# Performance work log

Hardware: AMD Instinct MI355X
Metric: run time of the kernel (lower is better)

## Reference

```python
import jax, jax.numpy as jnp
import numpy as np
from jax.ops import segment_sum, segment_max

N = 38332
E = 1200000
C = 64
POI_LEN = 38333
CAT_LEN = 400
LAYERS = 5


def _glorot(key, shape):
    fan_in, fan_out = shape[0], shape[-1]
    lim = float(np.sqrt(6.0 / (fan_in + fan_out)))
    return jax.random.uniform(key, shape, jnp.float32, -lim, lim)


def gcn_conv(x, src, dst, ew, W, b):
    # PyG GCNConv: x@W, add self-loops (weight 1), symmetric norm, scatter-sum at dst
    h = x @ W  # [N, Cout]
    ar = jnp.arange(N, dtype=src.dtype)
    s = jnp.concatenate([src, ar])
    d = jnp.concatenate([dst, ar])
    w = jnp.concatenate([ew, jnp.ones((N,), ew.dtype)])
    deg = segment_sum(w, d, num_segments=N)
    dinv = jnp.where(deg > 0, jax.lax.rsqrt(jnp.maximum(deg, 1e-12)), 0.0)
    norm = dinv[s] * w * dinv[d]
    out = segment_sum(h[s] * norm[:, None], d, num_segments=N)
    return out + b


def graph_norm(x, w, b, alpha, eps=1e-5):
    mean = jnp.mean(x, axis=0, keepdims=True)
    out = x - alpha * mean
    var = jnp.mean(out * out, axis=0, keepdims=True)
    return out * jax.lax.rsqrt(var + eps) * w + b


def gat_conv(x, src, dst, W, att_src, att_dst, b):
    # PyG GATConv, heads=1, add_self_loops=True, negative_slope=0.2
    h = x @ W  # [N, C]
    ar = jnp.arange(N, dtype=src.dtype)
    s = jnp.concatenate([src, ar])
    d = jnp.concatenate([dst, ar])
    a_s = h @ att_src  # [N]
    a_d = h @ att_dst
    e = jax.nn.leaky_relu(a_s[s] + a_d[d], 0.2)  # [E+N]
    m = segment_max(e, d, num_segments=N)
    ex = jnp.exp(e - m[d])
    z = segment_sum(ex, d, num_segments=N)
    alpha = ex / (z[d] + 1e-16)
    out = segment_sum(h[s] * alpha[:, None], d, num_segments=N)
    return out + b


def setup_inputs() -> dict:
    key = jax.random.key(0)
    ks = jax.random.split(key, 32)
    inp = {
        'poi_idx': jax.random.randint(ks[0], (N,), 0, POI_LEN, jnp.int32),
        'cat_idx': jax.random.randint(ks[1], (N,), 0, CAT_LEN, jnp.int32),
        'feat': jax.random.normal(ks[2], (N, 3), jnp.float32),
        'edge_index': jax.random.randint(ks[3], (2, E), 0, N, jnp.int32),
        'weight': jax.random.uniform(ks[4], (E,), jnp.float32),
        'poi_emb': jax.random.normal(ks[5], (POI_LEN, 300), jnp.float32),
        'cat_emb': jax.random.normal(ks[6], (CAT_LEN, 100), jnp.float32),
        'W_in': _glorot(ks[7], (403, C)),
        'b_in': jnp.zeros((C,), jnp.float32),
        'gcn_W': jax.vmap(lambda k: _glorot(k, (C, C)))(jax.random.split(ks[8], LAYERS)),
        'gcn_b': jnp.zeros((LAYERS, C), jnp.float32),
        'gn_w': jnp.ones((LAYERS, C), jnp.float32),
        'gn_b': jnp.zeros((LAYERS, C), jnp.float32),
        'gn_a': jnp.ones((LAYERS, C), jnp.float32),
        'gat_W': jax.vmap(lambda k: _glorot(k, (C, C)))(jax.random.split(ks[9], LAYERS)),
        'gat_att_src': jax.random.normal(ks[10], (LAYERS, C), jnp.float32) * 0.1,
        'gat_att_dst': jax.random.normal(ks[11], (LAYERS, C), jnp.float32) * 0.1,
        'gat_b': jnp.zeros((LAYERS, C), jnp.float32),
        'W_out': _glorot(ks[12], (C, 1)),
        'b_out': jnp.zeros((1,), jnp.float32),
        'fc1_W': _glorot(ks[13], (N, 128)),
        'fc1_b': jnp.zeros((128,), jnp.float32),
        'fc2_W': _glorot(ks[14], (128, POI_LEN)),
        'fc2_b': jnp.zeros((POI_LEN,), jnp.float32),
    }
    return inp


def reference(poi_idx, cat_idx, feat, edge_index, weight, poi_emb, cat_emb,
              W_in, b_in, gcn_W, gcn_b, gn_w, gn_b, gn_a,
              gat_W, gat_att_src, gat_att_dst, gat_b,
              W_out, b_out, fc1_W, fc1_b, fc2_W, fc2_b):
    src, dst = edge_index[0], edge_index[1]
    lrelu = lambda v: jax.nn.leaky_relu(v, 0.01)  # nn.LeakyReLU default
    x = jnp.concatenate([poi_emb[poi_idx], cat_emb[cat_idx], feat], axis=1)  # [N,403]
    x = lrelu(gcn_conv(x, src, dst, weight, W_in, b_in))  # [N,64]
    for i in range(LAYERS):
        t = gcn_conv(x, src, dst, weight, gcn_W[i], gcn_b[i])
        t = lrelu(graph_norm(t, gn_w[i], gn_b[i], gn_a[i]))
        x = x + t
        t = gat_conv(x, src, dst, gat_W[i], gat_att_src[i], gat_att_dst[i], gat_b[i])
        t = lrelu(graph_norm(t, gn_w[i], gn_b[i], gn_a[i]))
        x = x + t
    x = lrelu(gcn_conv(x, src, dst, weight, W_out, b_out)).reshape(-1)  # [N]
    h = jax.nn.relu(x @ fc1_W + fc1_b)
    out = jax.nn.relu(h @ fc2_W + fc2_b)  # [POI_LEN]
    return out
```

## Files before the change

### kernel.cpp

```cpp
#include <hip/hip_runtime.h>
#include <hip/hip_fp16.h>

#define NN 38332
#define NE 1200000
#define POI 38333
#define NWG 128
#define CHUNK (NE/NWG)
#define SBLK 256
#define FBLK 1024

__device__ __forceinline__ float lrelu01(float v){ return v > 0.f ? v : 0.01f*v; }

__device__ __forceinline__ void load8(const __half* h, int s, int c8, float* f){
  uint4 q = *(const uint4*)((const __half*)h + (size_t)s*64 + c8);
  __half2 h0 = *(__half2*)&q.x, h1 = *(__half2*)&q.y, h2 = *(__half2*)&q.z, h3 = *(__half2*)&q.w;
  float2 r0 = __half22float2(h0), r1 = __half22float2(h1), r2 = __half22float2(h2), r3 = __half22float2(h3);
  f[0]=r0.x; f[1]=r0.y; f[2]=r1.x; f[3]=r1.y; f[4]=r2.x; f[5]=r2.y; f[6]=r3.x; f[7]=r3.y;
}
__device__ __forceinline__ void load8(const float* h, int s, int c8, float* f){
  float4 a = *(const float4*)(h + (size_t)s*64 + c8);
  float4 b = *(const float4*)(h + (size_t)s*64 + c8 + 4);
  f[0]=a.x; f[1]=a.y; f[2]=a.z; f[3]=a.w; f[4]=b.x; f[5]=b.y; f[6]=b.z; f[7]=b.w;
}
__device__ __forceinline__ void store8(float* out, int n, int cb, const float* o){
  *(float4*)&out[(size_t)n*64 + cb]     = make_float4(o[0],o[1],o[2],o[3]);
  *(float4*)&out[(size_t)n*64 + cb + 4] = make_float4(o[4],o[5],o[6],o[7]);
}
__device__ __forceinline__ void store8(__half* out, int n, int cb, const float* o){
  __half2 q0 = __floats2half2_rn(o[0], o[1]);
  __half2 q1 = __floats2half2_rn(o[2], o[3]);
  __half2 q2 = __floats2half2_rn(o[4], o[5]);
  __half2 q3 = __floats2half2_rn(o[6], o[7]);
  uint4 q;
  q.x = *(unsigned*)&q0; q.y = *(unsigned*)&q1; q.z = *(unsigned*)&q2; q.w = *(unsigned*)&q3;
  *(uint4*)((__half*)out + (size_t)n*64 + cb) = q;
}

__global__ __launch_bounds__(1024) void k_hist(const int* __restrict__ dst,
                                               int* __restrict__ partial){
  __shared__ int hist[NN];
  for (int i = threadIdx.x; i < NN; i += 1024) hist[i] = 0;
  __syncthreads();
  int base = blockIdx.x*CHUNK;
  for (int k = threadIdx.x; k < CHUNK; k += 1024)
    atomicAdd(&hist[dst[base + k]], 1);
  __syncthreads();
  for (int i = threadIdx.x; i < NN; i += 1024)
    partial[(size_t)blockIdx.x*NN + i] = hist[i];
}

__global__ __launch_bounds__(256) void k_b1(int* __restrict__ partial, int* __restrict__ counts){
  int bin = blockIdx.x*256 + threadIdx.x;
  if (bin < NN){
    int run = 0;
    for (int wg = 0; wg < NWG; ++wg){
      int v = partial[(size_t)wg*NN + bin];
      partial[(size_t)wg*NN + bin] = run;
      run += v;
    }
    counts[bin] = run;
  }
}

__global__ __launch_bounds__(1024) void k_scan(const int* __restrict__ counts, int* rowptr){
  __shared__ int part[1024];
  int tid = threadIdx.x;
  const int per = (NN + 1023)/1024;
  int base = tid*per;
  int s = 0;
  for (int k = 0; k < per; k++){ int i = base + k; if (i < NN) s += counts[i]; }
  part[tid] = s;
  __syncthreads();
  for (int off = 1; off < 1024; off <<= 1){
    int v = (tid >= off) ? part[tid-off] : 0;
    __syncthreads();
    part[tid] += v;
    __syncthreads();
  }
  int run = (tid == 0) ? 0 : part[tid-1];
  for (int k = 0; k < per; k++){
    int i = base + k;
    if (i < NN){ rowptr[i] = run; run += counts[i]; }
  }
  if (tid == 1023) rowptr[NN] = run;
}

__global__ __launch_bounds__(1024) void k_scatter(const int* __restrict__ src,
                                                  const int* __restrict__ dst,
                                                  const float* __restrict__ ew,
                                                  const int* __restrict__ rowptr,
                                                  const int* __restrict__ partial,
                                                  int2* __restrict__ cw){
  __shared__ int cur[NN];
  for (int i = threadIdx.x; i < NN; i += 1024)
    cur[i] = rowptr[i] + partial[(size_t)blockIdx.x*NN + i];
  __syncthreads();
  int base = blockIdx.x*CHUNK;
  for (int k = threadIdx.x; k < CHUNK; k += 1024){
    int e = base + k;
    int d = dst[e];
    int pos = atomicAdd(&cur[d], 1);
    cw[pos] = make_int2(src[e], __float_as_int(ew[e]));
  }
}

__global__ __launch_bounds__(256) void k_dinv(const int* __restrict__ rowptr,
                                              const int2* __restrict__ cw,
                                              float* __restrict__ dinv){
  int lane = threadIdx.x & 63;
  int n = blockIdx.x*4 + (threadIdx.x >> 6);
  int beg = rowptr[n], end = rowptr[n+1];
  float s = 0.f;
  for (int e = beg + lane; e < end; e += 64) s += __int_as_float(cw[e].y);
  #pragma unroll
  for (int off = 32; off; off >>= 1) s += __shfl_xor(s, off);
  if (lane == 0) dinv[n] = rsqrtf(1.0f + s);
}

__global__ __launch_bounds__(256) void k_scale(const int* __restrict__ rowptr,
                                               const float* __restrict__ dinv,
                                               int2* __restrict__ cw){
  int lane = threadIdx.x & 63;
  int n = blockIdx.x*4 + (threadIdx.x >> 6);
  float dn = dinv[n];
  int beg = rowptr[n], end = rowptr[n+1];
  for (int e = beg + lane; e < end; e += 64){
    int2 p = cw[e];
    cw[e].y = __float_as_int(dinv[p.x]*__int_as_float(p.y)*dn);
  }
}

template<int K>
__global__ __launch_bounds__(256) void k_proj(const float* __restrict__ emb,
                                              const float* __restrict__ W,
                                              float* __restrict__ outp, int rows){
  int lane = threadIdx.x & 63;
  int base = __builtin_amdgcn_readfirstlane(blockIdx.x*32 + (threadIdx.x >> 6)*8);
  float acc[8] = {0.f,0.f,0.f,0.f,0.f,0.f,0.f,0.f};
  constexpr int NCH = (K + 63)/64;
  #pragma unroll
  for (int ch = 0; ch < NCH; ++ch){
    float Wreg[64];
    #pragma unroll
    for (int j = 0; j < 64; ++j)
      Wreg[j] = (ch*64 + j < K) ? W[(ch*64 + j)*64 + lane] : 0.f;
    #pragma unroll
    for (int r = 0; r < 8; ++r){
      int row = base + r;
      if (row < rows){
        const float* er = emb + (size_t)row*K + ch*64;
        #pragma unroll
        for (int j = 0; j < 64; ++j)
          if (ch*64 + j < K) acc[r] = fmaf(er[j], Wreg[j], acc[r]);
      }
    }
  }
  #pragma unroll
  for (int r = 0; r < 8; ++r){
    int row = base + r;
    if (row < rows) outp[(size_t)row*64 + lane] = acc[r];
  }
}

__global__ __launch_bounds__(256) void k_gather(const int* __restrict__ poi_idx,
                                                const int* __restrict__ cat_idx,
                                                const float* __restrict__ feat,
                                                const float* __restrict__ pproj,
                                                const float* __restrict__ cproj,
                                                const float* __restrict__ Wf,
                                                float* __restrict__ outh){
  int i = blockIdx.x*256 + threadIdx.x;
  int n = i >> 6, c = i & 63;
  float f0 = feat[n*3], f1 = feat[n*3+1], f2 = feat[n*3+2];
  float v = pproj[(size_t)poi_idx[n]*64 + c] + cproj[(size_t)cat_idx[n]*64 + c];
  v = fmaf(f0, Wf[c], v);
  v = fmaf(f1, Wf[64 + c], v);
  v = fmaf(f2, Wf[128 + c], v);
  outh[i] = v;
}

template<bool ATT, bool RESID>
__global__ __launch_bounds__(256) void k_lin64f(float* __restrict__ x,
                                                const __half* __restrict__ t,
                                                const float* __restrict__ stats,
                                                const float* __restrict__ gb,
                                                const float* __restrict__ W,
                                                const float* __restrict__ att_src,
                                                const float* __restrict__ att_dst,
                                                __half* __restrict__ h,
                                                float* __restrict__ a_s,
                                                float* __restrict__ a_d){
  int lane = threadIdx.x & 63;
  int base = blockIdx.x*32 + (threadIdx.x >> 6)*8;
  float Wreg[64];
  #pragma unroll
  for (int j = 0; j < 64; ++j) Wreg[j] = W[j*64 + lane];
  float coef = 0.f, shift = 0.f, gbv = 0.f;
  if (RESID){
    coef  = stats[128 + lane];
    shift = stats[192 + lane];
    gbv   = gb[lane];
  }
  float as_l = 0.f, ad_l = 0.f;
  if (ATT){ as_l = att_src[lane]; ad_l = att_dst[lane]; }
  #pragma unroll
  for (int r = 0; r < 8; ++r){
    int row = base + r;
    if (row < NN){
      float xn = x[(size_t)row*64 + lane];
      if (RESID){
        float tv = __half2float(t[(size_t)row*64 + lane]);
        xn += lrelu01((tv - shift)*coef + gbv);
        x[(size_t)row*64 + lane] = xn;
      }
      int xi = __float_as_int(xn);
      float acc = 0.f;
      #pragma unroll
      for (int j = 0; j < 64; ++j)
        acc = fmaf(__int_as_float(__builtin_amdgcn_readlane(xi, j)), Wreg[j], acc);
      h[(size_t)row*64 + lane] = __float2half(acc);
      if (ATT){
        float s1 = acc*as_l, s2 = acc*ad_l;
        #pragma unroll
        for (int off = 32; off; off >>= 1){ s1 += __shfl_xor(s1, off); s2 += __shfl_xor(s2, off); }
        if (lane == 0){ a_s[row] = s1; a_d[row] = s2; }
      }
    }
  }
}

template<bool DO_LRELU, typename TIN, typename TOUT>
__global__ __launch_bounds__(256) void k_gcn_prop(const TIN* __restrict__ h,
                                                  const int* __restrict__ rowptr,
                                                  const int2* __restrict__ cw,
                                                  const float* __restrict__ dinv,
                                                  const float* __restrict__ bias,
                                                  TOUT* __restrict__ out){
  int lane = threadIdx.x & 63;
  int n = __builtin_amdgcn_readfirstlane(blockIdx.x*4 + (threadIdx.x >> 6));
  int beg = rowptr[n], end = rowptr[n+1];
  int deg = end - beg;
  int g  = lane >> 3;
  int c8 = (lane & 7) << 3;
  float acc[8] = {0.f,0.f,0.f,0.f,0.f,0.f,0.f,0.f};
  if (deg < 64){
    int sv = n; float wv = 0.f;
    if (lane < deg){
      int2 p = cw[beg + lane];
      sv = p.x; wv = __int_as_float(p.y);
    } else if (lane == deg){
      float di = dinv[n];
      wv = di*di;
    }
    int ne = deg + 1;
    int nit = (ne + 7) >> 3;
    float w0 = __shfl(wv, g);
    int  sj0 = __shfl(sv, g);
    float f0[8]; load8(h, sj0, c8, f0);
    for (int it = 1; it < nit; ++it){
      int ei = (it << 3) + g;
      float w1 = __shfl(wv, ei);
      int  sj1 = __shfl(sv, ei);
      float f1[8]; load8(h, sj1, c8, f1);
      #pragma unroll
      for (int j = 0; j < 8; ++j) acc[j] = fmaf(w0, f0[j], acc[j]);
      w0 = w1;
      #pragma unroll
      for (int j = 0; j < 8; ++j) f0[j] = f1[j];
    }
    #pragma unroll
    for (int j = 0; j < 8; ++j) acc[j] = fmaf(w0, f0[j], acc[j]);
  } else {
    {
      float di = dinv[n];
      float w = (g == 0) ? di*di : 0.f;
      float f[8]; load8(h, n, c8, f);
      #pragma unroll
      for (int j = 0; j < 8; ++j) acc[j] = fmaf(w, f[j], acc[j]);
    }
    int nit = (deg + 7) >> 3;
    for (int it = 0; it < nit; ++it){
      int ei = (it << 3) + g;
      int2 p = cw[beg + (ei < deg ? ei : 0)];
      float w = (ei < deg) ? __int_as_float(p.y) : 0.f;
      float f[8]; load8(h, p.x, c8, f);
      #pragma unroll
      for (int j = 0; j < 8; ++j) acc[j] = fmaf(w, f[j], acc[j]);
    }
  }
  #pragma unroll
  for (int m = 8; m < 64; m <<= 1){
    #pragma unroll
    for (int j = 0; j < 8; ++j) acc[j] += __shfl_xor(acc[j], m);
  }
  if (lane < 8){
    int cb = lane << 3;
    float4 b0 = *(const float4*)&bias[cb];
    float4 b1 = *(const float4*)&bias[cb + 4];
    float o[8] = {acc[0]+b0.x, acc[1]+b0.y, acc[2]+b0.z, acc[3]+b0.w,
                  acc[4]+b1.x, acc[5]+b1.y, acc[6]+b1.z, acc[7]+b1.w};
    if (DO_LRELU){
      #pragma unroll
      for (int j = 0; j < 8; ++j) o[j] = lrelu01(o[j]);
    }
    store8(out, n, cb, o);
  }
}

__global__ __launch_bounds__(256) void k_gat_prop(const __half* __restrict__ h,
                                                  const int* __restrict__ rowptr,
                                                  const int2* __restrict__ cw,
                                                  const float* __restrict__ a_s,
                                                  const float* __restrict__ a_d,
                                                  const float* __restrict__ bias,
                                                  __half* __restrict__ out){
  int lane = threadIdx.x & 63;
  int n = __builtin_amdgcn_readfirstlane(blockIdx.x*4 + (threadIdx.x >> 6));
  int beg = rowptr[n], end = rowptr[n+1];
  int deg = end - beg;
  float ad = a_d[n];
  float se = a_s[n] + ad; se = se > 0.f ? se : 0.2f*se;
  if (deg <= 64){
    int s = 0; float v = -1e30f;
    if (lane < deg){
      s = cw[beg + lane].x;
      v = a_s[s] + ad; v = v > 0.f ? v : 0.2f*v;
    }
    float m = fmaxf(se, v);
    #pragma unroll
    for (int off = 32; off; off >>= 1) m = fmaxf(m, __shfl_xor(m, off));
    float ev = (lane < deg) ? __expf(v - m) : 0.f;
    float z = ev;
    #pragma unroll
    for (int off = 32; off; off >>= 1) z += __shfl_xor(z, off);
    float es = __expf(se - m);
    z += es;
    float zinv = 1.0f/(z + 1e-16f);
    int g = lane >> 3, c8 = (lane & 7) << 3;
    float acc[8] = {0.f,0.f,0.f,0.f,0.f,0.f,0.f,0.f};
    { float f[8]; load8(h, n, c8, f);
      float w = (g == 0) ? es : 0.f;
      #pragma unroll
      for (int j = 0; j < 8; ++j) acc[j] = fmaf(w, f[j], acc[j]);
    }
    int nit = (deg + 7) >> 3;
    if (nit > 0){
      float w0 = __shfl(ev, g);
      int  sj0 = __shfl(s,  g);
      float f0[8]; load8(h, sj0, c8, f0);
      for (int it = 1; it < nit; ++it){
        int ei = (it << 3) + g;
        float w1 = __shfl(ev, ei);
        int  sj1 = __shfl(s,  ei);
        float f1[8]; load8(h, sj1, c8, f1);
        #pragma unroll
        for (int j = 0; j < 8; ++j) acc[j] = fmaf(w0, f0[j], acc[j]);
        w0 = w1;
        #pragma unroll
        for (int j = 0; j < 8; ++j) f0[j] = f1[j];
      }
      #pragma unroll
      for (int j = 0; j < 8; ++j) acc[j] = fmaf(w0, f0[j], acc[j]);
    }
    #pragma unroll
    for (int mm = 8; mm < 64; mm <<= 1){
      #pragma unroll
      for (int j = 0; j < 8; ++j) acc[j] += __shfl_xor(acc[j], mm);
    }
    if (lane < 8){
      int cb = lane << 3;
      float4 b0 = *(const float4*)&bias[cb];
      float4 b1 = *(const float4*)&bias[cb + 4];
      float o[8] = {fmaf(acc[0],zinv,b0.x), fmaf(acc[1],zinv,b0.y), fmaf(acc[2],zinv,b0.z), fmaf(acc[3],zinv,b0.w),
                    fmaf(acc[4],zinv,b1.x), fmaf(acc[5],zinv,b1.y), fmaf(acc[6],zinv,b1.z), fmaf(acc[7],zinv,b1.w)};
      store8(out, n, cb, o);
    }
  } else {
    float m = se;
    for (int e = beg + lane; e < end; e += 64){
      float v = a_s[cw[e].x] + ad; v = v > 0.f ? v : 0.2f*v;
      m = fmaxf(m, v);
    }
    #pragma unroll
    for (int off = 32; off; off >>= 1) m = fmaxf(m, __shfl_xor(m, off));
    float z = 0.f;
    for (int e = beg + lane; e < end; e += 64){
      float v = a_s[cw[e].x] + ad; v = v > 0.f ? v : 0.2f*v;
      z += __expf(v - m);
    }
    #pragma unroll
    for (int off = 32; off; off >>= 1) z += __shfl_xor(z, off);
    float es = __expf(se - m);
    z += es;
    float zinv = 1.0f/(z + 1e-16f);
    float acc = es*(float)h[(size_t)n*64 + lane];
    for (int e = beg; e < end; ++e){
      int sj = cw[e].x;
      float v = a_s[sj] + ad; v = v > 0.f ? v : 0.2f*v;
      acc = fmaf(__expf(v - m), (float)h[(size_t)sj*64 + lane], acc);
    }
    out[(size_t)n*64 + lane] = __float2half(acc*zinv + bias[lane]);
  }
}

__global__ __launch_bounds__(256) void k_colstats(const __half* __restrict__ t,
                                                  float* __restrict__ pstats){
  int lane = threadIdx.x & 63;
  int sub  = threadIdx.x >> 6;
  float s = 0.f, s2 = 0.f;
  for (int n = blockIdx.x*4 + sub; n < NN; n += gridDim.x*4){
    float v = __half2float(t[(size_t)n*64 + lane]);
    s += v; s2 = fmaf(v, v, s2);
  }
  __shared__ float ls[256], ls2[256];
  ls[threadIdx.x] = s; ls2[threadIdx.x] = s2;
  __syncthreads();
  if (threadIdx.x < 64){
    s  = ls[threadIdx.x]  + ls[threadIdx.x+64]  + ls[threadIdx.x+128]  + ls[threadIdx.x+192];
    s2 = ls2[threadIdx.x] + ls2[threadIdx.x+64] + ls2[threadIdx.x+128] + ls2[threadIdx.x+192];
    pstats[blockIdx.x*128 + threadIdx.x]      = s;
    pstats[blockIdx.x*128 + 64 + threadIdx.x] = s2;
  }
}

__global__ __launch_bounds__(256) void k_chan(const float* __restrict__ pstats,
                                              const float* __restrict__ gw,
                                              const float* __restrict__ ga,
                                              float* __restrict__ stats){
  int lane = threadIdx.x & 63, w = threadIdx.x >> 6;
  float s = 0.f, s2 = 0.f;
  for (int blk = w*(SBLK/4); blk < (w+1)*(SBLK/4); ++blk){
    s  += pstats[blk*128 + lane];
    s2 += pstats[blk*128 + 64 + lane];
  }
  __shared__ float ls[256], ls2[256];
  ls[threadIdx.x] = s; ls2[threadIdx.x] = s2;
  __syncthreads();
  if (threadIdx.x < 64){
    int c = threadIdx.x;
    s  = ls[c]  + ls[c+64]  + ls[c+128]  + ls[c+192];
    s2 = ls2[c] + ls2[c+64] + ls2[c+128] + ls2[c+192];
    const float invN = 1.0f/(float)NN;
    float m  = s*invN, ms = s2*invN, a = ga[c];
    float var = ms - m*m*a*(2.0f - a);
    stats[128 + c] = rsqrtf(var + 1e-5f)*gw[c];
    stats[192 + c] = a*m;
  }
}

__global__ __launch_bounds__(256) void k_outlinf(const float* __restrict__ x,
                                                 const __half* __restrict__ t,
                                                 const float* __restrict__ stats,
                                                 const float* __restrict__ gb,
                                                 const float* __restrict__ Wout,
                                                 float* __restrict__ h1){
  int lane = threadIdx.x & 63, wave = threadIdx.x >> 6;
  int n = blockIdx.x*4 + wave;
  float coef  = stats[128 + lane];
  float shift = stats[192 + lane];
  float xn = x[(size_t)n*64 + lane];
  float tv = __half2float(t[(size_t)n*64 + lane]);
  xn += lrelu01((tv - shift)*coef + gb[lane]);
  float v = xn*Wout[lane];
  #pragma unroll
  for (int off = 32; off; off >>= 1) v += __shfl_xor(v, off);
  if (lane == 0) h1[n] = v;
}

__global__ __launch_bounds__(256) void k_prop1(const float* __restrict__ h1,
                                               const int* __restrict__ rowptr,
                                               const int2* __restrict__ cw,
                                               const float* __restrict__ dinv,
                                               const float* __restrict__ b_out,
                                               float* __restrict__ xs){
  int lane = threadIdx.x & 63;
  int n = blockIdx.x*32 + (threadIdx.x >> 6)*8 + (lane >> 3);
  bool ok = n < NN;
  int beg = ok ? rowptr[n] : 0;
  int end = ok ? rowptr[n+1] : 0;
  float acc = 0.f;
  for (int e = beg + (lane & 7); e < end; e += 8){
    int2 p = cw[e];
    acc = fmaf(__int_as_float(p.y), h1[p.x], acc);
  }
  acc += __shfl_xor(acc, 1);
  acc += __shfl_xor(acc, 2);
  acc += __shfl_xor(acc, 4);
  if (ok && (lane & 7) == 0){
    float di = dinv[n];
    xs[n] = lrelu01(acc + di*di*h1[n] + b_out[0]);
  }
}

__global__ __launch_bounds__(256) void k_fc1(const float* __restrict__ xs,
                                             const float* __restrict__ W,
                                             float* __restrict__ pfc){
  int j = threadIdx.x & 127, half = threadIdx.x >> 7;
  float acc = 0.f;
  for (int n = blockIdx.x*2 + half; n < NN; n += gridDim.x*2)
    acc = fmaf(xs[n], W[(size_t)n*128 + j], acc);
  __shared__ float ls[256];
  ls[threadIdx.x] = acc;
  __syncthreads();
  if (threadIdx.x < 128) pfc[blockIdx.x*128 + j] = ls[j] + ls[128 + j];
}

__global__ __launch_bounds__(256) void k_fcr(const float* __restrict__ pfc,
                                             const float* __restrict__ fc1_b,
                                             float* __restrict__ hfc){
  int j = blockIdx.x;
  int tid = threadIdx.x;
  float acc = 0.f;
  #pragma unroll
  for (int k = 0; k < FBLK/256; ++k)
    acc += pfc[(size_t)(tid + k*256)*128 + j];
  __shared__ float ls[256];
  ls[tid] = acc;
  __syncthreads();
  for (int off = 128; off > 0; off >>= 1){
    if (tid < off) ls[tid] += ls[tid + off];
    __syncthreads();
  }
  if (tid == 0){
    float v = ls[0] + fc1_b[j];
    hfc[j] = v > 0.f ? v : 0.f;
  }
}

__global__ __launch_bounds__(256) void k_fc2(const float* __restrict__ hfc,
                                             const float* __restrict__ W2,
                                             const float* __restrict__ b2,
                                             float* __restrict__ out){
  __shared__ float hs[128];
  if (threadIdx.x < 128) hs[threadIdx.x] = hfc[threadIdx.x];
  __syncthreads();
  int p = blockIdx.x*64 + (threadIdx.x >> 2);
  int q = threadIdx.x & 3;
  if (p < POI){
    float acc = 0.f;
    #pragma unroll
    for (int j = q; j < 128; j += 4)
      acc = fmaf(hs[j], W2[(size_t)j*POI + p], acc);
    acc += __shfl_xor(acc, 1);
    acc += __shfl_xor(acc, 2);
    if (q == 0){
      float v = acc + b2[p];
      out[p] = v > 0.f ? v : 0.f;
    }
  }
}

extern "C" void kernel_launch(void* const* d_in, const int* in_sizes, int n_in,
                              void* d_out, int out_size, void* d_ws, size_t ws_size,
                              hipStream_t stream) {
  const int*   poi_idx = (const int*)d_in[0];
  const int*   cat_idx = (const int*)d_in[1];
  const float* feat    = (const float*)d_in[2];
  const int*   eidx    = (const int*)d_in[3];
  const int*   src     = eidx;
  const int*   dst     = eidx + NE;
  const float* ew      = (const float*)d_in[4];
  const float* poi_emb = (const float*)d_in[5];
  const float* cat_emb = (const float*)d_in[6];
  const float* W_in    = (const float*)d_in[7];
  const float* b_in    = (const float*)d_in[8];
  const float* gcn_W   = (const float*)d_in[9];
  const float* gcn_b   = (const float*)d_in[10];
  const float* gn_w    = (const float*)d_in[11];
  const float* gn_b    = (const float*)d_in[12];
  const float* gn_a    = (const float*)d_in[13];
  const float* gat_W   = (const float*)d_in[14];
  const float* att_s   = (const float*)d_in[15];
  const float* att_d   = (const float*)d_in[16];
  const float* gat_b   = (const float*)d_in[17];
  const float* W_out   = (const float*)d_in[18];
  const float* b_out   = (const float*)d_in[19];
  const float* fc1_W   = (const float*)d_in[20];
  const float* fc1_b   = (const float*)d_in[21];
  const float* fc2_W   = (const float*)d_in[22];
  const float* fc2_b   = (const float*)d_in[23];
  float* out = (float*)d_out;

  char* p = (char*)d_ws;
  auto alloc = [&](size_t bytes){ void* r = (void*)p; p += (bytes + 255) & ~(size_t)255; return r; };
  float*  x      = (float*) alloc((size_t)NN*64*4);
  float*  t32    = (float*) alloc((size_t)NN*64*4);
  __half* t      = (__half*)alloc((size_t)NN*64*2);
  __half* h      = (__half*)alloc((size_t)NN*64*2);
  int*    partial= (int*)   alloc((size_t)NWG*NN*4);
  float*  pproj  = (float*) partial;
  float*  cproj  = (float*) alloc((size_t)400*64*4);
  int2*   cw     = (int2*)  alloc((size_t)NE*8);
  float*  dinv   = (float*) alloc(NN*4);
  int*    counts = (int*)   alloc(NN*4);
  int*    rowptr = (int*)   alloc((NN+1)*4);
  float*  a_s    = (float*) alloc(NN*4);
  float*  a_d    = (float*) alloc(NN*4);
  float*  pstats = (float*) alloc((size_t)SBLK*128*4);
  float*  stats  = (float*) alloc(256*4);
  float*  h1     = (float*) alloc(NN*4);
  float*  xs     = (float*) alloc(NN*4);
  float*  pfc    = (float*) alloc((size_t)FBLK*128*4);
  float*  hfc    = (float*) alloc(128*4);

  const int G_N   = (NN + 255)/256;
  const int G_W4  = NN/4;
  const int G_L   = (NN + 31)/32;
  const int G_PJ  = (POI + 31)/32;
  const int G_EL  = NN*64/256;
  const int G_P1  = (NN + 31)/32;
  const int G_F2  = (POI + 63)/64;

  k_hist   <<<NWG, 1024, 0, stream>>>(dst, partial);
  k_b1     <<<G_N, 256, 0, stream>>>(partial, counts);
  k_scan   <<<1, 1024, 0, stream>>>(counts, rowptr);
  k_scatter<<<NWG, 1024, 0, stream>>>(src, dst, ew, rowptr, partial, cw);
  k_dinv   <<<G_W4, 256, 0, stream>>>(rowptr, cw, dinv);
  k_scale  <<<G_W4, 256, 0, stream>>>(rowptr, dinv, cw);

  k_proj<300><<<G_PJ, 256, 0, stream>>>(poi_emb, W_in, pproj, POI);
  k_proj<100><<<13, 256, 0, stream>>>(cat_emb, W_in + 300*64, cproj, 400);
  k_gather<<<G_EL, 256, 0, stream>>>(poi_idx, cat_idx, feat, pproj, cproj, W_in + 400*64, t32);
  k_gcn_prop<true, float, float><<<G_W4, 256, 0, stream>>>(t32, rowptr, cw, dinv, b_in, x);

  for (int i = 0; i < 5; i++){
    if (i == 0)
      k_lin64f<false,false><<<G_L, 256, 0, stream>>>(x, nullptr, nullptr, nullptr,
                                                     gcn_W, nullptr, nullptr, h, nullptr, nullptr);
    else
      k_lin64f<false,true><<<G_L, 256, 0, stream>>>(x, t, stats, gn_b + (i-1)*64,
                                                    gcn_W + i*4096, nullptr, nullptr, h, nullptr, nullptr);
    k_gcn_prop<false, __half, __half><<<G_W4, 256, 0, stream>>>(h, rowptr, cw, dinv, gcn_b + i*64, t);
    k_colstats<<<SBLK, 256, 0, stream>>>(t, pstats);
    k_chan<<<1, 256, 0, stream>>>(pstats, gn_w + i*64, gn_a + i*64, stats);
    k_lin64f<true,true><<<G_L, 256, 0, stream>>>(x, t, stats, gn_b + i*64,
                                                 gat_W + i*4096, att_s + i*64, att_d + i*64, h, a_s, a_d);
    k_gat_prop<<<G_W4, 256, 0, stream>>>(h, rowptr, cw, a_s, a_d, gat_b + i*64, t);
    k_colstats<<<SBLK, 256, 0, stream>>>(t, pstats);
    k_chan<<<1, 256, 0, stream>>>(pstats, gn_w + i*64, gn_a + i*64, stats);
  }

  k_outlinf<<<G_W4, 256, 0, stream>>>(x, t, stats, gn_b + 4*64, W_out, h1);
  k_prop1<<<G_P1, 256, 0, stream>>>(h1, rowptr, cw, dinv, b_out, xs);
  k_fc1<<<FBLK, 256, 0, stream>>>(xs, fc1_W, pfc);
  k_fcr<<<128, 256, 0, stream>>>(pfc, fc1_b, hfc);
  k_fc2<<<G_F2, 256, 0, stream>>>(hfc, fc2_W, fc2_b, out);
}
```

Baseline: 993.1 us.

## Double gather streams in propagation loops and shrink projection tiles

The low-degree paths of the GCN and GAT propagation kernels now process 16 neighbours per iteration using two independent accumulator sets, so more row gathers are in flight at once to hide memory latency. The embedding projection kernel now handles 4 rows per wave instead of 8, with more blocks launched. The histogram/scatter workgroup count also rises from 128 to 192. The costs are higher register pressure, an extra reduction step, and rereading the W weights more often in the projection.

```diff
diff --git a/kernel.cpp b/kernel.cpp
--- a/kernel.cpp
+++ b/kernel.cpp
@@ -4,7 +4,7 @@
 #define NN 38332
 #define NE 1200000
 #define POI 38333
-#define NWG 128
+#define NWG 192
 #define CHUNK (NE/NWG)
 #define SBLK 256
 #define FBLK 1024
@@ -135,8 +135,8 @@
                                               const float* __restrict__ W,
                                               float* __restrict__ outp, int rows){
   int lane = threadIdx.x & 63;
-  int base = __builtin_amdgcn_readfirstlane(blockIdx.x*32 + (threadIdx.x >> 6)*8);
-  float acc[8] = {0.f,0.f,0.f,0.f,0.f,0.f,0.f,0.f};
+  int base = __builtin_amdgcn_readfirstlane(blockIdx.x*16 + (threadIdx.x >> 6)*4);
+  float acc[4] = {0.f,0.f,0.f,0.f};
   constexpr int NCH = (K + 63)/64;
   #pragma unroll
   for (int ch = 0; ch < NCH; ++ch){
@@ -145,7 +145,7 @@
     for (int j = 0; j < 64; ++j)
       Wreg[j] = (ch*64 + j < K) ? W[(ch*64 + j)*64 + lane] : 0.f;
     #pragma unroll
-    for (int r = 0; r < 8; ++r){
+    for (int r = 0; r < 4; ++r){
       int row = base + r;
       if (row < rows){
         const float* er = emb + (size_t)row*K + ch*64;
@@ -156,7 +156,7 @@
     }
   }
   #pragma unroll
-  for (int r = 0; r < 8; ++r){
+  for (int r = 0; r < 4; ++r){
     int row = base + r;
     if (row < rows) outp[(size_t)row*64 + lane] = acc[r];
   }
@@ -243,6 +243,7 @@
   int g  = lane >> 3;
   int c8 = (lane & 7) << 3;
   float acc[8] = {0.f,0.f,0.f,0.f,0.f,0.f,0.f,0.f};
+  float acc2[8] = {0.f,0.f,0.f,0.f,0.f,0.f,0.f,0.f};
   if (deg < 64){
     int sv = n; float wv = 0.f;
     if (lane < deg){
@@ -253,23 +254,31 @@
       wv = di*di;
     }
     int ne = deg + 1;
-    int nit = (ne + 7) >> 3;
-    float w0 = __shfl(wv, g);
-    int  sj0 = __shfl(sv, g);
-    float f0[8]; load8(h, sj0, c8, f0);
+    int nit = (ne + 15) >> 4;
+    float wA0 = __shfl(wv, g),     wB0 = __shfl(wv, 8 + g);
+    int   sA0 = __shfl(sv, g),     sB0 = __shfl(sv, 8 + g);
+    float fA0[8], fB0[8];
+    load8(h, sA0, c8, fA0); load8(h, sB0, c8, fB0);
     for (int it = 1; it < nit; ++it){
-      int ei = (it << 3) + g;
-      float w1 = __shfl(wv, ei);
-      int  sj1 = __shfl(sv, ei);
-      float f1[8]; load8(h, sj1, c8, f1);
-      #pragma unroll
-      for (int j = 0; j < 8; ++j) acc[j] = fmaf(w0, f0[j], acc[j]);
-      w0 = w1;
-      #pragma unroll
-      for (int j = 0; j < 8; ++j) f0[j] = f1[j];
-    }
-    #pragma unroll
-    for (int j = 0; j < 8; ++j) acc[j] = fmaf(w0, f0[j], acc[j]);
+      int eiA = (it << 4) + g, eiB = eiA + 8;
+      float wA1 = __shfl(wv, eiA), wB1 = __shfl(wv, eiB);
+      int   sA1 = __shfl(sv, eiA), sB1 = __shfl(sv, eiB);
+      float fA1[8], fB1[8];
+      load8(h, sA1, c8, fA1); load8(h, sB1, c8, fB1);
+      #pragma unroll
+      for (int j = 0; j < 8; ++j){
+        acc[j]  = fmaf(wA0, fA0[j], acc[j]);
+        acc2[j] = fmaf(wB0, fB0[j], acc2[j]);
+      }
+      wA0 = wA1; wB0 = wB1;
+      #pragma unroll
+      for (int j = 0; j < 8; ++j){ fA0[j] = fA1[j]; fB0[j] = fB1[j]; }
+    }
+    #pragma unroll
+    for (int j = 0; j < 8; ++j){
+      acc[j]  = fmaf(wA0, fA0[j], acc[j]);
+      acc2[j] = fmaf(wB0, fB0[j], acc2[j]);
+    }
   } else {
     {
       float di = dinv[n];
@@ -288,6 +297,8 @@
       for (int j = 0; j < 8; ++j) acc[j] = fmaf(w, f[j], acc[j]);
     }
   }
+  #pragma unroll
+  for (int j = 0; j < 8; ++j) acc[j] += acc2[j];
   #pragma unroll
   for (int m = 8; m < 64; m <<= 1){
     #pragma unroll
@@ -338,30 +349,41 @@
     float zinv = 1.0f/(z + 1e-16f);
     int g = lane >> 3, c8 = (lane & 7) << 3;
     float acc[8] = {0.f,0.f,0.f,0.f,0.f,0.f,0.f,0.f};
+    float acc2[8] = {0.f,0.f,0.f,0.f,0.f,0.f,0.f,0.f};
     { float f[8]; load8(h, n, c8, f);
       float w = (g == 0) ? es : 0.f;
       #pragma unroll
       for (int j = 0; j < 8; ++j) acc[j] = fmaf(w, f[j], acc[j]);
     }
-    int nit = (deg + 7) >> 3;
+    int nit = (deg + 15) >> 4;
     if (nit > 0){
-      float w0 = __shfl(ev, g);
-      int  sj0 = __shfl(s,  g);
-      float f0[8]; load8(h, sj0, c8, f0);
+      float wA0 = __shfl(ev, g),     wB0 = __shfl(ev, 8 + g);
+      int   sA0 = __shfl(s,  g),     sB0 = __shfl(s,  8 + g);
+      float fA0[8], fB0[8];
+      load8(h, sA0, c8, fA0); load8(h, sB0, c8, fB0);
       for (int it = 1; it < nit; ++it){
-        int ei = (it << 3) + g;
-        float w1 = __shfl(ev, ei);
-        int  sj1 = __shfl(s,  ei);
-        float f1[8]; load8(h, sj1, c8, f1);
+        int eiA = (it << 4) + g, eiB = eiA + 8;
+        float wA1 = __shfl(ev, eiA), wB1 = __shfl(ev, eiB);
+        int   sA1 = __shfl(s,  eiA), sB1 = __shfl(s,  eiB);
+        float fA1[8], fB1[8];
+        load8(h, sA1, c8, fA1); load8(h, sB1, c8, fB1);
         #pragma unroll
-        for (int j = 0; j < 8; ++j) acc[j] = fmaf(w0, f0[j], acc[j]);
-        w0 = w1;
+        for (int j = 0; j < 8; ++j){
+          acc[j]  = fmaf(wA0, fA0[j], acc[j]);
+          acc2[j] = fmaf(wB0, fB0[j], acc2[j]);
+        }
+        wA0 = wA1; wB0 = wB1;
         #pragma unroll
-        for (int j = 0; j < 8; ++j) f0[j] = f1[j];
+        for (int j = 0; j < 8; ++j){ fA0[j] = fA1[j]; fB0[j] = fB1[j]; }
       }
       #pragma unroll
-      for (int j = 0; j < 8; ++j) acc[j] = fmaf(w0, f0[j], acc[j]);
-    }
+      for (int j = 0; j < 8; ++j){
+        acc[j]  = fmaf(wA0, fA0[j], acc[j]);
+        acc2[j] = fmaf(wB0, fB0[j], acc2[j]);
+      }
+    }
+    #pragma unroll
+    for (int j = 0; j < 8; ++j) acc[j] += acc2[j];
     #pragma unroll
     for (int mm = 8; mm < 64; mm <<= 1){
       #pragma unroll
@@ -606,7 +628,7 @@
   const int G_N   = (NN + 255)/256;
   const int G_W4  = NN/4;
   const int G_L   = (NN + 31)/32;
-  const int G_PJ  = (POI + 31)/32;
+  const int G_PJ  = (POI + 15)/16;
   const int G_EL  = NN*64/256;
   const int G_P1  = (NN + 31)/32;
   const int G_F2  = (POI + 63)/64;
@@ -619,7 +641,7 @@
   k_scale  <<<G_W4, 256, 0, stream>>>(rowptr, dinv, cw);
 
   k_proj<300><<<G_PJ, 256, 0, stream>>>(poi_emb, W_in, pproj, POI);
-  k_proj<100><<<13, 256, 0, stream>>>(cat_emb, W_in + 300*64, cproj, 400);
+  k_proj<100><<<25, 256, 0, stream>>>(cat_emb, W_in + 300*64, cproj, 400);
   k_gather<<<G_EL, 256, 0, stream>>>(poi_idx, cat_idx, feat, pproj, cproj, W_in + 400*64, t32);
   k_gcn_prop<true, float, float><<<G_W4, 256, 0, stream>>>(t32, rowptr, cw, dinv, b_in, x);
 
```

Result: faster. 969.6 us (-2.4%).
